# Performance work log

Measured on AMD Instinct MI355X. Metric: run time of the kernel, lower is better.

Reference implementation:

```python
import jax, jax.numpy as jnp
import numpy as np

EPS = 1e-12  # matches torch F.normalize default eps

def setup_inputs() -> dict:
    key = jax.random.key(0)
    k1, k2 = jax.random.split(key)
    x_pred = jax.random.normal(k1, (4, 4, 64, 64), dtype=jnp.float32)
    x_src = jax.random.normal(k2, (4, 4, 64, 64), dtype=jnp.float32)
    return {"x_pred": x_pred, "x_src": x_src}

def _l2_normalize_channels(z):
    # z: [B, C, N]; normalize along C (torch F.normalize: x / max(||x||, eps))
    norm = jnp.sqrt(jnp.sum(z * z, axis=1, keepdims=True))
    return z / jnp.maximum(norm, EPS)

def reference(x_pred, x_src):
    x_pred = x_pred.astype(jnp.float32)
    x_src = x_src.astype(jnp.float32)
    B, C, H, W = x_pred.shape
    N = H * W
    z_pred = _l2_normalize_channels(x_pred.reshape(B, C, N))
    z_src = _l2_normalize_channels(x_src.reshape(B, C, N))
    # Gram matrices: [B, N, N] cosine similarity between spatial positions
    A_pred = jnp.einsum('bcn,bcm->bnm', z_pred, z_pred)
    A_src = jnp.einsum('bcn,bcm->bnm', z_src, z_src)
    diff = A_pred - A_src
    loss = jnp.sum(diff * diff)
    loss = loss / (B * N * N)
    return loss
```

## Files before the change

### kernel.cpp

```cpp
#include <hip/hip_runtime.h>
#include <math.h>


#define NORM_EPS 1e-12f

__global__ __launch_bounds__(1024) void cosine_ssm_kernel(
    const float* __restrict__ x_pred,
    const float* __restrict__ x_src,
    float* __restrict__ out)
{
    constexpr int C = 4, N = 4096;
    const int b    = blockIdx.x;
    const int tid  = threadIdx.x;
    const int lane = tid & 63;
    const int wave = tid >> 6;

    const float* pb = x_pred + (size_t)b * C * N;
    const float* sb = x_src  + (size_t)b * C * N;

    float gu[10], gv[10], m[16];
#pragma unroll
    for (int i = 0; i < 10; ++i) { gu[i] = 0.f; gv[i] = 0.f; }
#pragma unroll
    for (int i = 0; i < 16; ++i) m[i] = 0.f;

    const int n0 = tid * 4;

    float pv[4][4], sv[4][4];
#pragma unroll
    for (int c = 0; c < C; ++c) {
        float4 t = *(const float4*)(pb + c * N + n0);
        pv[c][0] = t.x; pv[c][1] = t.y; pv[c][2] = t.z; pv[c][3] = t.w;
        float4 q = *(const float4*)(sb + c * N + n0);
        sv[c][0] = q.x; sv[c][1] = q.y; sv[c][2] = q.z; sv[c][3] = q.w;
    }

#pragma unroll
    for (int k = 0; k < 4; ++k) {
        float np = 0.f, ns = 0.f;
#pragma unroll
        for (int c = 0; c < 4; ++c) {
            np += pv[c][k] * pv[c][k];
            ns += sv[c][k] * sv[c][k];
        }
        const float ip = 1.f / fmaxf(sqrtf(np), NORM_EPS);
        const float is = 1.f / fmaxf(sqrtf(ns), NORM_EPS);
        float u[4], v[4];
#pragma unroll
        for (int c = 0; c < 4; ++c) { u[c] = pv[c][k] * ip; v[c] = sv[c][k] * is; }

        int idx = 0;
#pragma unroll
        for (int i = 0; i < 4; ++i)
#pragma unroll
            for (int j = i; j < 4; ++j) {
                gu[idx] += u[i] * u[j];
                gv[idx] += v[i] * v[j];
                ++idx;
            }
#pragma unroll
        for (int i = 0; i < 4; ++i)
#pragma unroll
            for (int j = 0; j < 4; ++j)
                m[i * 4 + j] += u[i] * v[j];
    }

    float acc[36];
#pragma unroll
    for (int i = 0; i < 10; ++i) { acc[i] = gu[i]; acc[10 + i] = gv[i]; }
#pragma unroll
    for (int i = 0; i < 16; ++i) acc[20 + i] = m[i];

#pragma unroll
    for (int off = 32; off >= 1; off >>= 1) {
#pragma unroll
        for (int i = 0; i < 36; ++i)
            acc[i] += __shfl_down(acc[i], off, 64);
    }

    __shared__ float lds[16][36];
    if (lane == 0) {
#pragma unroll
        for (int i = 0; i < 36; ++i) lds[wave][i] = acc[i];
    }
    __syncthreads();

    if (tid < 36) {
        float s = 0.f;
#pragma unroll
        for (int w = 0; w < 16; ++w) s += lds[w][tid];
        lds[0][tid] = s;
    }
    __syncthreads();

    if (tid == 0) {
        const float* g = &lds[0][0];
        const float fu = g[0]*g[0] + g[4]*g[4] + g[7]*g[7] + g[9]*g[9]
                       + 2.f*(g[1]*g[1] + g[2]*g[2] + g[3]*g[3] + g[5]*g[5] + g[6]*g[6] + g[8]*g[8]);
        const float* h = &lds[0][10];
        const float fv = h[0]*h[0] + h[4]*h[4] + h[7]*h[7] + h[9]*h[9]
                       + 2.f*(h[1]*h[1] + h[2]*h[2] + h[3]*h[3] + h[5]*h[5] + h[6]*h[6] + h[8]*h[8]);
        const float* mm = &lds[0][20];
        float fm = 0.f;
#pragma unroll
        for (int i = 0; i < 16; ++i) fm += mm[i] * mm[i];

        const float contrib = (fu + fv - 2.f * fm) * (1.0f / (4.0f * 4096.0f * 4096.0f));
        atomicAdd(out, contrib);
    }
}

extern "C" void kernel_launch(void* const* d_in, const int* in_sizes, int n_in,
                              void* d_out, int out_size, void* d_ws, size_t ws_size,
                              hipStream_t stream) {
    const float* x_pred = (const float*)d_in[0];
    const float* x_src  = (const float*)d_in[1];
    float* out = (float*)d_out;

    hipMemsetAsync(out, 0, sizeof(float), stream);
    cosine_ssm_kernel<<<4, 1024, 0, stream>>>(x_pred, x_src, out);
}
```

Baseline: 65.73 us.

## Split Gram-stat reduction into 64 single-wave blocks plus finalize kernel

Replaces the 4-block, 1024-thread kernel with 64 single-wave blocks that each write 36 partial statistics to workspace. A second one-block kernel sums the partials per batch and computes the loss. This drops the memset and the atomicAdd. The aim is to spread the loads across more CUs and shorten the in-block LDS reduction, at the cost of an extra kernel launch and a workspace round trip.

Result: faster. 59.54 us (-9.4%).

```diff
diff --git a/kernel.cpp b/kernel.cpp
--- a/kernel.cpp
+++ b/kernel.cpp
@@ -4,27 +4,20 @@
 
 #define NORM_EPS 1e-12f
 
-__global__ __launch_bounds__(1024) void cosine_ssm_kernel(
+__global__ __launch_bounds__(64) void cosine_ssm_partial(
     const float* __restrict__ x_pred,
     const float* __restrict__ x_src,
-    float* __restrict__ out)
+    float* __restrict__ ws)
 {
     constexpr int C = 4, N = 4096;
-    const int b    = blockIdx.x;
-    const int tid  = threadIdx.x;
-    const int lane = tid & 63;
-    const int wave = tid >> 6;
+    const int slot = blockIdx.x;
+    const int b    = slot >> 4;
+    const int s    = slot & 15;
+    const int lane = threadIdx.x;
 
     const float* pb = x_pred + (size_t)b * C * N;
     const float* sb = x_src  + (size_t)b * C * N;
-
-    float gu[10], gv[10], m[16];
-#pragma unroll
-    for (int i = 0; i < 10; ++i) { gu[i] = 0.f; gv[i] = 0.f; }
-#pragma unroll
-    for (int i = 0; i < 16; ++i) m[i] = 0.f;
-
-    const int n0 = tid * 4;
+    const int n0 = s * 256 + lane * 4;
 
     float pv[4][4], sv[4][4];
 #pragma unroll
@@ -34,6 +27,10 @@
         float4 q = *(const float4*)(sb + c * N + n0);
         sv[c][0] = q.x; sv[c][1] = q.y; sv[c][2] = q.z; sv[c][3] = q.w;
     }
+
+    float acc[36];
+#pragma unroll
+    for (int i = 0; i < 36; ++i) acc[i] = 0.f;
 
 #pragma unroll
     for (int k = 0; k < 4; ++k) {
@@ -54,22 +51,16 @@
         for (int i = 0; i < 4; ++i)
 #pragma unroll
             for (int j = i; j < 4; ++j) {
-                gu[idx] += u[i] * u[j];
-                gv[idx] += v[i] * v[j];
+                acc[idx]      += u[i] * u[j];
+                acc[10 + idx] += v[i] * v[j];
                 ++idx;
             }
 #pragma unroll
         for (int i = 0; i < 4; ++i)
 #pragma unroll
             for (int j = 0; j < 4; ++j)
-                m[i * 4 + j] += u[i] * v[j];
+                acc[20 + i * 4 + j] += u[i] * v[j];
     }
-
-    float acc[36];
-#pragma unroll
-    for (int i = 0; i < 10; ++i) { acc[i] = gu[i]; acc[10 + i] = gv[i]; }
-#pragma unroll
-    for (int i = 0; i < 16; ++i) acc[20 + i] = m[i];
 
 #pragma unroll
     for (int off = 32; off >= 1; off >>= 1) {
@@ -78,35 +69,50 @@
             acc[i] += __shfl_down(acc[i], off, 64);
     }
 
-    __shared__ float lds[16][36];
     if (lane == 0) {
 #pragma unroll
-        for (int i = 0; i < 36; ++i) lds[wave][i] = acc[i];
+        for (int i = 0; i < 36; ++i)
+            ws[i * 64 + slot] = acc[i];
+    }
+}
+
+__global__ __launch_bounds__(192) void cosine_ssm_finalize(
+    const float* __restrict__ ws,
+    float* __restrict__ out)
+{
+    __shared__ float g[4][36];
+    __shared__ float contrib[4];
+    const int t = threadIdx.x;
+
+    if (t < 144) {
+        const int b = t / 36;
+        const int i = t - b * 36;
+        const float* src = ws + i * 64 + b * 16;
+        float ssum = 0.f;
+#pragma unroll
+        for (int s = 0; s < 16; ++s) ssum += src[s];
+        g[b][i] = ssum;
     }
     __syncthreads();
 
-    if (tid < 36) {
-        float s = 0.f;
+    if (t < 4) {
+        const float* a = g[t];
+        const float fu = a[0]*a[0] + a[4]*a[4] + a[7]*a[7] + a[9]*a[9]
+                       + 2.f*(a[1]*a[1] + a[2]*a[2] + a[3]*a[3] + a[5]*a[5] + a[6]*a[6] + a[8]*a[8]);
+        const float* h = a + 10;
+        const float fv = h[0]*h[0] + h[4]*h[4] + h[7]*h[7] + h[9]*h[9]
+                       + 2.f*(h[1]*h[1] + h[2]*h[2] + h[3]*h[3] + h[5]*h[5] + h[6]*h[6] + h[8]*h[8]);
+        const float* mm = a + 20;
+        float fm = 0.f;
 #pragma unroll
-        for (int w = 0; w < 16; ++w) s += lds[w][tid];
-        lds[0][tid] = s;
+        for (int i = 0; i < 16; ++i) fm += mm[i] * mm[i];
+        contrib[t] = fu + fv - 2.f * fm;
     }
     __syncthreads();
 
-    if (tid == 0) {
-        const float* g = &lds[0][0];
-        const float fu = g[0]*g[0] + g[4]*g[4] + g[7]*g[7] + g[9]*g[9]
-                       + 2.f*(g[1]*g[1] + g[2]*g[2] + g[3]*g[3] + g[5]*g[5] + g[6]*g[6] + g[8]*g[8]);
-        const float* h = &lds[0][10];
-        const float fv = h[0]*h[0] + h[4]*h[4] + h[7]*h[7] + h[9]*h[9]
-                       + 2.f*(h[1]*h[1] + h[2]*h[2] + h[3]*h[3] + h[5]*h[5] + h[6]*h[6] + h[8]*h[8]);
-        const float* mm = &lds[0][20];
-        float fm = 0.f;
-#pragma unroll
-        for (int i = 0; i < 16; ++i) fm += mm[i] * mm[i];
-
-        const float contrib = (fu + fv - 2.f * fm) * (1.0f / (4.0f * 4096.0f * 4096.0f));
-        atomicAdd(out, contrib);
+    if (t == 0) {
+        const float scale = 1.0f / (4.0f * 4096.0f * 4096.0f);
+        out[0] = (contrib[0] + contrib[1] + contrib[2] + contrib[3]) * scale;
     }
 }
 
@@ -115,8 +121,9 @@
                               hipStream_t stream) {
     const float* x_pred = (const float*)d_in[0];
     const float* x_src  = (const float*)d_in[1];
+    float* ws  = (float*)d_ws;
     float* out = (float*)d_out;
 
-    hipMemsetAsync(out, 0, sizeof(float), stream);
-    cosine_ssm_kernel<<<4, 1024, 0, stream>>>(x_pred, x_src, out);
+    cosine_ssm_partial<<<64, 64, 0, stream>>>(x_pred, x_src, ws);
+    cosine_ssm_finalize<<<1, 192, 0, stream>>>(ws, out);
 }
```
